# Kernel tuning notes

Hardware: AMD Instinct MI355X
Metric: run time of the kernel (lower is better)

Reference implementation:

```python
import jax, jax.numpy as jnp
import numpy as np
import math

B, S, D, H = 2, 2048, 1024, 16
DK = D // H


def setup_inputs() -> dict:
    key = jax.random.key(0)
    ks = jax.random.split(key, 12)
    s = 0.02
    return {
        "query": jax.random.normal(ks[0], (B, S, D), jnp.float32),
        "key": jax.random.normal(ks[1], (B, S, D), jnp.float32),
        "value": jax.random.normal(ks[2], (B, S, D), jnp.float32),
        "mask": jnp.zeros((1, 1, S, S), jnp.float32),
        "Wq": jax.random.normal(ks[3], (D, D), jnp.float32) * s,
        "bq": jnp.zeros((D,), jnp.float32),
        "Wk": jax.random.normal(ks[4], (D, D), jnp.float32) * s,
        "bk": jnp.zeros((D,), jnp.float32),
        "Wv": jax.random.normal(ks[5], (D, D), jnp.float32) * s,
        "bv": jnp.zeros((D,), jnp.float32),
        "Wpost": jax.random.normal(ks[6], (D, D), jnp.float32) * s,
        "bpost": jnp.zeros((D,), jnp.float32),
        "per_dim_scale": jnp.zeros((DK,), jnp.float32),
    }


def reference(query, key, value, mask, Wq, bq, Wk, bk, Wv, bv, Wpost, bpost, per_dim_scale):
    # Linear projections (torch Linear: x @ W.T + b), split heads -> [B, H, S, DK]
    def proj(x, W, b):
        return (x @ W.T + b).reshape(B, S, H, DK).transpose(0, 2, 1, 3)

    q = proj(query, Wq, bq)
    k = proj(key, Wk, bk)
    v = proj(value, Wv, bv)

    # PerDimScale: scale = (1/ln2) / sqrt(d_k) * softplus(per_dim_scale)
    r_softplus_0 = 1.442695041
    scale = (r_softplus_0 / math.sqrt(DK)) * jax.nn.softplus(per_dim_scale)
    q = q * scale  # broadcast over last dim

    # Full attention matrix [B, H, S, S] + additive mask + softmax (dropout p=0)
    attn = jnp.einsum('bhqd,bhkd->bhqk', q, k) + mask
    attn = jax.nn.softmax(attn, axis=-1)

    out = jnp.einsum('bhqk,bhkd->bhqd', attn, v)
    out = out.transpose(0, 2, 1, 3).reshape(B, S, D)
    return out @ Wpost.T + bpost
```

## Files before the change

kernel.cpp:

```cpp
#include <hip/hip_runtime.h>
#include <math.h>

typedef __bf16 bf16;
typedef __bf16 bf16x8 __attribute__((ext_vector_type(8)));
typedef float f32x4 __attribute__((ext_vector_type(4)));

static constexpr int NB = 2, NS = 2048, ND = 1024, NH = 16, NDK = 64;
static constexpr float LOG2E = 1.442695041f;

__device__ __forceinline__ f32x4 mfma16(bf16x8 a, bf16x8 b, f32x4 c) {
  return __builtin_amdgcn_mfma_f32_16x16x32_bf16(a, b, c, 0, 0, 0);
}

__device__ __forceinline__ float exp2_fast(float x) {
  return __builtin_amdgcn_exp2f(x);
}

__device__ __forceinline__ void gload16(const void* g, void* l) {
  __builtin_amdgcn_global_load_lds(
      (const __attribute__((address_space(1))) void*)g,
      (__attribute__((address_space(3))) void*)l, 16, 0, 0);
}

__global__ void scale_kernel(const float* __restrict__ pds, float* __restrict__ scale) {
  int i = threadIdx.x;
  if (i < NDK) {
    float x = pds[i];
    float sp = fmaxf(x, 0.0f) + log1pf(expf(-fabsf(x)));
    scale[i] = (LOG2E * LOG2E / 8.0f) * sp;
  }
}

__global__ void maskflag_kernel(const float* __restrict__ mask, int* __restrict__ flag, int n4) {
  int idx = blockIdx.x * blockDim.x + threadIdx.x;
  int stride = gridDim.x * blockDim.x;
  unsigned acc = 0;
  for (int i = idx; i < n4; i += stride) {
    float4 v = ((const float4*)mask)[i];
    acc |= (__float_as_uint(v.x) << 1) | (__float_as_uint(v.y) << 1)
         | (__float_as_uint(v.z) << 1) | (__float_as_uint(v.w) << 1);
  }
  if (acc != 0) atomicOr(flag, 1);
}

__global__ __launch_bounds__(256) void cvt_bf16(
    const float* __restrict__ s0, const float* __restrict__ s1,
    const float* __restrict__ s2, const float* __restrict__ s3,
    bf16* __restrict__ d0, bf16* __restrict__ d1,
    bf16* __restrict__ d2, bf16* __restrict__ d3, int n8) {
  const float* s = blockIdx.y == 0 ? s0 : blockIdx.y == 1 ? s1 : blockIdx.y == 2 ? s2 : s3;
  bf16* d = blockIdx.y == 0 ? d0 : blockIdx.y == 1 ? d1 : blockIdx.y == 2 ? d2 : d3;
  for (int i = blockIdx.x * 256 + threadIdx.x; i < n8; i += gridDim.x * 256) {
    const float4* f = (const float4*)s + 2 * (size_t)i;
    float4 a = f[0], b = f[1];
    bf16x8 o;
    o[0] = (bf16)a.x; o[1] = (bf16)a.y; o[2] = (bf16)a.z; o[3] = (bf16)a.w;
    o[4] = (bf16)b.x; o[5] = (bf16)b.y; o[6] = (bf16)b.z; o[7] = (bf16)b.w;
    *((bf16x8*)d + i) = o;
  }
}

__global__ __launch_bounds__(256) void qkv_mm(
    const bf16* __restrict__ Xq, const bf16* __restrict__ Xk, const bf16* __restrict__ Xv,
    const bf16* __restrict__ Wqb, const bf16* __restrict__ Wkb, const bf16* __restrict__ Wvb,
    const float* __restrict__ bq, const float* __restrict__ bk, const float* __restrict__ bv,
    const float* __restrict__ scale2,
    bf16* __restrict__ Qs, bf16* __restrict__ Ks, bf16* __restrict__ Vt, int mode0) {
  __shared__ __align__(16) bf16 la[128 * 64];
  __shared__ __align__(16) bf16 lb[128 * 64];
  const int which = mode0 + blockIdx.y;
  const bf16* A  = which == 0 ? Xq  : which == 1 ? Xk  : Wvb;
  const bf16* Bm = which == 0 ? Wqb : which == 1 ? Wkb : Xv;
  const int t = threadIdx.x, lane = t & 63, wave = t >> 6;
  const int wm = wave >> 1, wn = wave & 1;
  int bm, bn;
  if (which == 2) { bm = blockIdx.x & 7; bn = blockIdx.x >> 3; }
  else            { bm = blockIdx.x >> 3; bn = blockIdx.x & 7; }
  const int g = lane >> 4, l15 = lane & 15;
  const int sr = wave * 8 + (lane >> 3);
  const int sc = ((lane & 7) ^ (lane >> 3)) * 8;
  const bf16* Abase = A  + (size_t)(bm * 128) * ND;
  const bf16* Bbase = Bm + (size_t)(bn * 128) * ND;

  f32x4 acc[4][4] = {};

  for (int kt = 0; kt < ND; kt += 64) {
    for (int c = 0; c < 4; ++c) {
      gload16(Abase + (size_t)(c * 32 + sr) * ND + kt + sc, la + c * 2048 + wave * 512);
      gload16(Bbase + (size_t)(c * 32 + sr) * ND + kt + sc, lb + c * 2048 + wave * 512);
    }
    __syncthreads();
    __builtin_amdgcn_s_setprio(1);
    for (int kk = 0; kk < 2; ++kk) {
      bf16x8 af[4], bfv[4];
      for (int m = 0; m < 4; ++m) {
        const int rr = wm * 64 + m * 16 + l15;
        af[m] = *(const bf16x8*)&la[rr * 64 + (((g + 4 * kk) ^ (rr & 7)) << 3)];
      }
      for (int n = 0; n < 4; ++n) {
        const int rr = wn * 64 + n * 16 + l15;
        bfv[n] = *(const bf16x8*)&lb[rr * 64 + (((g + 4 * kk) ^ (rr & 7)) << 3)];
      }
      for (int m = 0; m < 4; ++m)
        for (int n = 0; n < 4; ++n)
          acc[m][n] = mfma16(af[m], bfv[n], acc[m][n]);
    }
    __builtin_amdgcn_s_setprio(0);
    __syncthreads();
  }

  const int lr4 = g * 4;
  if (which != 2) {
    const float* bias = which ? bk : bq;
    bf16* outp = which ? Ks : Qs;
    for (int m = 0; m < 4; ++m) {
      const int grow0 = bm * 128 + wm * 64 + m * 16 + lr4;
      for (int n = 0; n < 4; ++n) {
        const int gcol = bn * 128 + wn * 64 + n * 16 + l15;
        const int h = gcol >> 6, dk = gcol & 63;
        const float bia = bias[gcol];
        const float sc2 = which ? 1.0f : scale2[dk];
        for (int r = 0; r < 4; ++r) {
          const int grow = grow0 + r;
          float v = acc[m][n][r] + bia;
          if (which == 0) v *= sc2;
          const int bb = grow >> 11, s = grow & (NS - 1);
          outp[(((size_t)(bb * NH + h)) * NS + s) * NDK + dk] = (bf16)v;
        }
      }
    }
  } else {
    for (int m = 0; m < 4; ++m) {
      const int d0 = bm * 128 + wm * 64 + m * 16 + lr4;
      for (int n = 0; n < 4; ++n) {
        const int gcol = bn * 128 + wn * 64 + n * 16 + l15;
        const int bb = gcol >> 11, s = gcol & (NS - 1);
        for (int r = 0; r < 4; ++r) {
          const int d = d0 + r;
          const float v = acc[m][n][r] + bv[d];
          const int h = d >> 6, dk = d & 63;
          Vt[(((size_t)(bb * NH + h)) * NDK + dk) * NS + s] = (bf16)v;
        }
      }
    }
  }
}

__global__ __launch_bounds__(256) void post_mm2(
    const bf16* __restrict__ A, const bf16* __restrict__ Bm,
    const float* __restrict__ bias, float* __restrict__ out) {
  __shared__ __align__(16) bf16 la[2][64 * 64];
  __shared__ __align__(16) bf16 lb[2][128 * 64];
  const int t = threadIdx.x, lane = t & 63, wave = t >> 6;
  const int bm = blockIdx.x >> 3, bn = blockIdx.x & 7;
  const int g = lane >> 4, l15 = lane & 15;
  const int sr = wave * 8 + (lane >> 3);
  const int sc = ((lane & 7) ^ (lane >> 3)) * 8;
  const bf16* Abase = A  + (size_t)(bm * 64) * ND;
  const bf16* Bbase = Bm + (size_t)(bn * 128) * ND;

  f32x4 acc[4][2] = {};

  auto stage = [&](int kt, int b) {
    for (int c = 0; c < 2; ++c)
      gload16(Abase + (size_t)(c * 32 + sr) * ND + kt + sc, la[b] + c * 2048 + wave * 512);
    for (int c = 0; c < 4; ++c)
      gload16(Bbase + (size_t)(c * 32 + sr) * ND + kt + sc, lb[b] + c * 2048 + wave * 512);
  };

  stage(0, 0);
  asm volatile("s_waitcnt vmcnt(0)" ::: "memory");
  __builtin_amdgcn_s_barrier();

  for (int it = 0; it < 16; ++it) {
    const int cur = it & 1;
    if (it + 1 < 16) stage((it + 1) * 64, cur ^ 1);

    __builtin_amdgcn_s_setprio(1);
    for (int kk = 0; kk < 2; ++kk) {
      bf16x8 af[4], bfv[2];
      for (int m = 0; m < 4; ++m) {
        const int rr = m * 16 + l15;
        af[m] = *(const bf16x8*)&la[cur][rr * 64 + (((g + 4 * kk) ^ (rr & 7)) << 3)];
      }
      for (int n = 0; n < 2; ++n) {
        const int rr = wave * 32 + n * 16 + l15;
        bfv[n] = *(const bf16x8*)&lb[cur][rr * 64 + (((g + 4 * kk) ^ (rr & 7)) << 3)];
      }
      for (int m = 0; m < 4; ++m)
        for (int n = 0; n < 2; ++n)
          acc[m][n] = mfma16(af[m], bfv[n], acc[m][n]);
    }
    __builtin_amdgcn_s_setprio(0);

    asm volatile("s_waitcnt vmcnt(0)" ::: "memory");
    __builtin_amdgcn_s_barrier();
  }

  for (int m = 0; m < 4; ++m) {
    const int grow0 = bm * 64 + m * 16 + g * 4;
    for (int n = 0; n < 2; ++n) {
      const int gcol = bn * 128 + wave * 32 + n * 16 + l15;
      const float bia = bias[gcol];
      for (int r = 0; r < 4; ++r)
        out[(size_t)(grow0 + r) * ND + gcol] = acc[m][n][r] + bia;
    }
  }
}

__global__ __launch_bounds__(256) void attn4(
    const bf16* __restrict__ Qs, const bf16* __restrict__ Ks,
    const bf16* __restrict__ Vt, const float* __restrict__ mask,
    const int* __restrict__ flag, bf16* __restrict__ Obs) {
  __shared__ __align__(16) bf16 lk[2][64 * 64];
  __shared__ __align__(16) bf16 lv[2][64 * 64];
  __shared__ __align__(16) bf16 lp[4][16 * 64];

  const int t = threadIdx.x, lane = t & 63, wave = t >> 6;
  const int g = lane >> 4, l15 = lane & 15;
  const int bh = blockIdx.y;
  const int qbase = blockIdx.x * 64 + wave * 16;
  const bool use_mask = (*flag) != 0;

  const bf16* Qh = Qs + (size_t)bh * NS * NDK;
  const bf16* Kh = Ks + (size_t)bh * NS * NDK;
  const bf16* Vh = Vt + (size_t)bh * NDK * NS;

  bf16x8 qf[2];
  for (int kk = 0; kk < 2; ++kk)
    qf[kk] = *(const bf16x8*)&Qh[(size_t)(qbase + l15) * NDK + kk * 32 + g * 8];

  f32x4 o_acc[4] = {};
  float lsum[4] = {0.0f, 0.0f, 0.0f, 0.0f};

  const int sr = wave * 8 + (lane >> 3);
  const int sc = ((lane & 7) ^ (lane >> 3)) * 8;

  auto stage = [&](int kv, int b) {
    for (int c = 0; c < 2; ++c) {
      gload16(Kh + (size_t)(kv + c * 32 + sr) * NDK + sc, lk[b] + c * 2048 + wave * 512);
      gload16(Vh + (size_t)(c * 32 + sr) * NS + kv + sc, lv[b] + c * 2048 + wave * 512);
    }
  };

  stage(0, 0);
  asm volatile("s_waitcnt vmcnt(0)" ::: "memory");
  __builtin_amdgcn_s_barrier();

  for (int kv = 0; kv < NS; kv += 64) {
    const int cur = (kv >> 6) & 1;
    if (kv + 64 < NS) stage(kv + 64, cur ^ 1);

    f32x4 sacc[4] = {};
    __builtin_amdgcn_s_setprio(1);
    for (int kk = 0; kk < 2; ++kk)
      for (int n = 0; n < 4; ++n) {
        const int rr = n * 16 + l15;
        bf16x8 kf = *(const bf16x8*)&lk[cur][rr * 64 + (((g + 4 * kk) ^ (rr & 7)) << 3)];
        sacc[n] = mfma16(qf[kk], kf, sacc[n]);
      }
    __builtin_amdgcn_s_setprio(0);

    if (use_mask) {
      for (int n = 0; n < 4; ++n)
        for (int r = 0; r < 4; ++r)
          sacc[n][r] += LOG2E * mask[(size_t)(qbase + g * 4 + r) * NS + kv + n * 16 + l15];
    }

    for (int n = 0; n < 4; ++n) {
      const int k = n * 16 + l15;
      for (int r = 0; r < 4; ++r) {
        const float e = exp2_fast(sacc[n][r]);
        lsum[r] += e;
        const int q = g * 4 + r;
        lp[wave][q * 64 + (k ^ ((q & 7) << 3))] = (bf16)e;
      }
    }

    for (int kk = 0; kk < 2; ++kk) {
      bf16x8 pf = *(const bf16x8*)&lp[wave][l15 * 64 + ((kk * 32 + g * 8) ^ ((l15 & 7) << 3))];
      __builtin_amdgcn_s_setprio(1);
      for (int n = 0; n < 4; ++n) {
        const int rr = n * 16 + l15;
        bf16x8 vf = *(const bf16x8*)&lv[cur][rr * 64 + (((g + 4 * kk) ^ (rr & 7)) << 3)];
        o_acc[n] = mfma16(pf, vf, o_acc[n]);
      }
      __builtin_amdgcn_s_setprio(0);
    }

    asm volatile("s_waitcnt vmcnt(0)" ::: "memory");
    __builtin_amdgcn_s_barrier();
  }

  const int bidx = bh >> 4, h = bh & 15;
  for (int r = 0; r < 4; ++r) {
    float rs = lsum[r];
    rs += __shfl_xor(rs, 1, 64);
    rs += __shfl_xor(rs, 2, 64);
    rs += __shfl_xor(rs, 4, 64);
    rs += __shfl_xor(rs, 8, 64);
    const float rinv = 1.0f / rs;
    const int qrow = qbase + g * 4 + r;
    for (int n = 0; n < 4; ++n)
      Obs[((size_t)(bidx * NS + qrow)) * ND + h * 64 + n * 16 + l15] = (bf16)(o_acc[n][r] * rinv);
  }
}

extern "C" void kernel_launch(void* const* d_in, const int* in_sizes, int n_in,
                              void* d_out, int out_size, void* d_ws, size_t ws_size,
                              hipStream_t stream) {
  (void)in_sizes; (void)n_in; (void)out_size;
  const float* query = (const float*)d_in[0];
  const float* key   = (const float*)d_in[1];
  const float* value = (const float*)d_in[2];
  const float* mask  = (const float*)d_in[3];
  const float* Wq    = (const float*)d_in[4];
  const float* bq    = (const float*)d_in[5];
  const float* Wk    = (const float*)d_in[6];
  const float* bk    = (const float*)d_in[7];
  const float* Wv    = (const float*)d_in[8];
  const float* bv    = (const float*)d_in[9];
  const float* Wpost = (const float*)d_in[10];
  const float* bpost = (const float*)d_in[11];
  const float* pds   = (const float*)d_in[12];

  char* ws = (char*)d_ws;
  const size_t MB = 1u << 20;
  bf16* Xq  = (bf16*)(ws + 0 * MB);
  bf16* Xk  = (bf16*)(ws + 8 * MB);
  bf16* Xv  = (bf16*)(ws + 16 * MB);
  bf16* Wqb = (bf16*)(ws + 24 * MB);
  bf16* Wkb = (bf16*)(ws + 26 * MB);
  bf16* Wvb = (bf16*)(ws + 28 * MB);
  bf16* Wpb = (bf16*)(ws + 30 * MB);
  float* scale2 = (float*)(ws + 32 * MB);
  int* flag     = (int*)(ws + 32 * MB + 256);

  const bool fused = ws_size >= (size_t)50 * MB;
  bf16 *Qsp, *Ksp, *Vtp, *Obsp;
  if (fused) {
    Qsp = (bf16*)d_out;
    Ksp = (bf16*)((char*)d_out + 8 * MB);
    Vtp = (bf16*)(ws + 33 * MB);
    Obsp = (bf16*)(ws + 41 * MB);
  } else {
    Qsp = (bf16*)d_out;
    Ksp = Xq;
    Vtp = Xk;
    Obsp = Xv;
  }

  (void)hipMemsetAsync(flag, 0, sizeof(int), stream);
  scale_kernel<<<1, 64, 0, stream>>>(pds, scale2);
  maskflag_kernel<<<256, 256, 0, stream>>>(mask, flag, NS * NS / 4);

  cvt_bf16<<<dim3(512, 3), 256, 0, stream>>>(query, key, value, nullptr,
                                             Xq, Xk, Xv, nullptr, NB * NS * ND / 8);
  cvt_bf16<<<dim3(512, 4), 256, 0, stream>>>(Wq, Wk, Wv, Wpost,
                                             Wqb, Wkb, Wvb, Wpb, ND * ND / 8);

  if (fused) {
    qkv_mm<<<dim3(256, 3), 256, 0, stream>>>(Xq, Xk, Xv, Wqb, Wkb, Wvb,
                                             bq, bk, bv, scale2, Qsp, Ksp, Vtp, 0);
  } else {
    qkv_mm<<<dim3(256, 1), 256, 0, stream>>>(Xq, Xk, Xv, Wqb, Wkb, Wvb,
                                             bq, bk, bv, scale2, Qsp, Ksp, Vtp, 0);
    qkv_mm<<<dim3(256, 1), 256, 0, stream>>>(Xq, Xk, Xv, Wqb, Wkb, Wvb,
                                             bq, bk, bv, scale2, Qsp, Ksp, Vtp, 1);
    qkv_mm<<<dim3(256, 1), 256, 0, stream>>>(Xq, Xk, Xv, Wqb, Wkb, Wvb,
                                             bq, bk, bv, scale2, Qsp, Ksp, Vtp, 2);
  }

  attn4<<<dim3(32, 32), 256, 0, stream>>>(Qsp, Ksp, Vtp, mask, flag, Obsp);

  post_mm2<<<512, 256, 0, stream>>>(Obsp, Wpb, bpost, (float*)d_out);
}
```

Baseline: 148.7 us.

## Double attention block to eight waves sharing K/V tiles, precompute LDS offsets

The attention kernel now runs 512 threads per block covering 128 query rows, so each staged 64-row K/V tile is shared by eight waves instead of four. That halves the global K/V traffic per query, and each wave issues one async load per buffer instead of two. Swizzled LDS offsets are precomputed into registers, loops are fully unrolled, and the KV loop is manually unrolled by two so the buffer index is a constant. The cost is higher register pressure, fewer blocks for the grid (512), and larger per-block barrier synchronisation.

```diff
diff --git a/kernel.cpp b/kernel.cpp
--- a/kernel.cpp
+++ b/kernel.cpp
@@ -208,18 +208,18 @@
   }
 }
 
-__global__ __launch_bounds__(256) void attn4(
+__global__ __launch_bounds__(512) void attn5(
     const bf16* __restrict__ Qs, const bf16* __restrict__ Ks,
     const bf16* __restrict__ Vt, const float* __restrict__ mask,
     const int* __restrict__ flag, bf16* __restrict__ Obs) {
-  __shared__ __align__(16) bf16 lk[2][64 * 64];
-  __shared__ __align__(16) bf16 lv[2][64 * 64];
-  __shared__ __align__(16) bf16 lp[4][16 * 64];
+  __shared__ __align__(16) bf16 lk[2 * 64 * 64];
+  __shared__ __align__(16) bf16 lv[2 * 64 * 64];
+  __shared__ __align__(16) bf16 lp[8 * 16 * 64];
 
   const int t = threadIdx.x, lane = t & 63, wave = t >> 6;
   const int g = lane >> 4, l15 = lane & 15;
   const int bh = blockIdx.y;
-  const int qbase = blockIdx.x * 64 + wave * 16;
+  const int qbase = blockIdx.x * 128 + wave * 16;
   const bool use_mask = (*flag) != 0;
 
   const bf16* Qh = Qs + (size_t)bh * NS * NDK;
@@ -227,72 +227,94 @@
   const bf16* Vh = Vt + (size_t)bh * NDK * NS;
 
   bf16x8 qf[2];
+#pragma unroll
   for (int kk = 0; kk < 2; ++kk)
     qf[kk] = *(const bf16x8*)&Qh[(size_t)(qbase + l15) * NDK + kk * 32 + g * 8];
 
   f32x4 o_acc[4] = {};
   float lsum[4] = {0.0f, 0.0f, 0.0f, 0.0f};
 
-  const int sr = wave * 8 + (lane >> 3);
+  unsigned kfo[2][4];
+#pragma unroll
+  for (int kk = 0; kk < 2; ++kk)
+#pragma unroll
+    for (int n = 0; n < 4; ++n)
+      kfo[kk][n] = (unsigned)((n * 16 + l15) * 64 + (((g + 4 * kk) ^ (l15 & 7)) << 3));
+  unsigned pwo[4][4];
+#pragma unroll
+  for (int n = 0; n < 4; ++n)
+#pragma unroll
+    for (int r = 0; r < 4; ++r) {
+      const int q = g * 4 + r;
+      pwo[n][r] = (unsigned)(wave * 1024 + q * 64 + ((n * 16 + l15) ^ ((q & 7) << 3)));
+    }
+  unsigned pro[2];
+#pragma unroll
+  for (int kk = 0; kk < 2; ++kk)
+    pro[kk] = (unsigned)(wave * 1024 + l15 * 64 + ((kk * 32 + g * 8) ^ ((l15 & 7) << 3)));
+
+  const int srow = wave * 8 + (lane >> 3);
   const int sc = ((lane & 7) ^ (lane >> 3)) * 8;
 
   auto stage = [&](int kv, int b) {
-    for (int c = 0; c < 2; ++c) {
-      gload16(Kh + (size_t)(kv + c * 32 + sr) * NDK + sc, lk[b] + c * 2048 + wave * 512);
-      gload16(Vh + (size_t)(c * 32 + sr) * NS + kv + sc, lv[b] + c * 2048 + wave * 512);
-    }
+    gload16(Kh + (size_t)(kv + srow) * NDK + sc, lk + b * 4096 + wave * 512);
+    gload16(Vh + (size_t)srow * NS + kv + sc, lv + b * 4096 + wave * 512);
+  };
+
+  auto body = [&](int kv, int cur) {
+    if (kv + 64 < NS) stage(kv + 64, cur ^ 1);
+
+    f32x4 sacc[4] = {};
+    __builtin_amdgcn_s_setprio(1);
+#pragma unroll
+    for (int kk = 0; kk < 2; ++kk)
+#pragma unroll
+      for (int n = 0; n < 4; ++n)
+        sacc[n] = mfma16(qf[kk], *(const bf16x8*)&lk[cur * 4096 + kfo[kk][n]], sacc[n]);
+    __builtin_amdgcn_s_setprio(0);
+
+    if (use_mask) {
+#pragma unroll
+      for (int n = 0; n < 4; ++n)
+#pragma unroll
+        for (int r = 0; r < 4; ++r)
+          sacc[n][r] += LOG2E * mask[(size_t)(qbase + g * 4 + r) * NS + kv + n * 16 + l15];
+    }
+
+#pragma unroll
+    for (int n = 0; n < 4; ++n)
+#pragma unroll
+      for (int r = 0; r < 4; ++r) {
+        const float e = exp2_fast(sacc[n][r]);
+        lsum[r] += e;
+        lp[pwo[n][r]] = (bf16)e;
+      }
+
+#pragma unroll
+    for (int kk = 0; kk < 2; ++kk) {
+      const bf16x8 pf = *(const bf16x8*)&lp[pro[kk]];
+      __builtin_amdgcn_s_setprio(1);
+#pragma unroll
+      for (int n = 0; n < 4; ++n)
+        o_acc[n] = mfma16(pf, *(const bf16x8*)&lv[cur * 4096 + kfo[kk][n]], o_acc[n]);
+      __builtin_amdgcn_s_setprio(0);
+    }
+
+    asm volatile("s_waitcnt vmcnt(0)" ::: "memory");
+    __builtin_amdgcn_s_barrier();
   };
 
   stage(0, 0);
   asm volatile("s_waitcnt vmcnt(0)" ::: "memory");
   __builtin_amdgcn_s_barrier();
 
-  for (int kv = 0; kv < NS; kv += 64) {
-    const int cur = (kv >> 6) & 1;
-    if (kv + 64 < NS) stage(kv + 64, cur ^ 1);
-
-    f32x4 sacc[4] = {};
-    __builtin_amdgcn_s_setprio(1);
-    for (int kk = 0; kk < 2; ++kk)
-      for (int n = 0; n < 4; ++n) {
-        const int rr = n * 16 + l15;
-        bf16x8 kf = *(const bf16x8*)&lk[cur][rr * 64 + (((g + 4 * kk) ^ (rr & 7)) << 3)];
-        sacc[n] = mfma16(qf[kk], kf, sacc[n]);
-      }
-    __builtin_amdgcn_s_setprio(0);
-
-    if (use_mask) {
-      for (int n = 0; n < 4; ++n)
-        for (int r = 0; r < 4; ++r)
-          sacc[n][r] += LOG2E * mask[(size_t)(qbase + g * 4 + r) * NS + kv + n * 16 + l15];
-    }
-
-    for (int n = 0; n < 4; ++n) {
-      const int k = n * 16 + l15;
-      for (int r = 0; r < 4; ++r) {
-        const float e = exp2_fast(sacc[n][r]);
-        lsum[r] += e;
-        const int q = g * 4 + r;
-        lp[wave][q * 64 + (k ^ ((q & 7) << 3))] = (bf16)e;
-      }
-    }
-
-    for (int kk = 0; kk < 2; ++kk) {
-      bf16x8 pf = *(const bf16x8*)&lp[wave][l15 * 64 + ((kk * 32 + g * 8) ^ ((l15 & 7) << 3))];
-      __builtin_amdgcn_s_setprio(1);
-      for (int n = 0; n < 4; ++n) {
-        const int rr = n * 16 + l15;
-        bf16x8 vf = *(const bf16x8*)&lv[cur][rr * 64 + (((g + 4 * kk) ^ (rr & 7)) << 3)];
-        o_acc[n] = mfma16(pf, vf, o_acc[n]);
-      }
-      __builtin_amdgcn_s_setprio(0);
-    }
-
-    asm volatile("s_waitcnt vmcnt(0)" ::: "memory");
-    __builtin_amdgcn_s_barrier();
+  for (int kv = 0; kv < NS; kv += 128) {
+    body(kv, 0);
+    body(kv + 64, 1);
   }
 
   const int bidx = bh >> 4, h = bh & 15;
+#pragma unroll
   for (int r = 0; r < 4; ++r) {
     float rs = lsum[r];
     rs += __shfl_xor(rs, 1, 64);
@@ -301,6 +323,7 @@
     rs += __shfl_xor(rs, 8, 64);
     const float rinv = 1.0f / rs;
     const int qrow = qbase + g * 4 + r;
+#pragma unroll
     for (int n = 0; n < 4; ++n)
       Obs[((size_t)(bidx * NS + qrow)) * ND + h * 64 + n * 16 + l15] = (bf16)(o_acc[n][r] * rinv);
   }
@@ -371,7 +394,7 @@
                                              bq, bk, bv, scale2, Qsp, Ksp, Vtp, 2);
   }
 
-  attn4<<<dim3(32, 32), 256, 0, stream>>>(Qsp, Ksp, Vtp, mask, flag, Obsp);
+  attn5<<<dim3(16, 32), 512, 0, stream>>>(Qsp, Ksp, Vtp, mask, flag, Obsp);
 
   post_mm2<<<512, 256, 0, stream>>>(Obsp, Wpb, bpost, (float*)d_out);
 }
```

Result: faster. 136.1 us (-8.5%).
